# Optimization experiments

Measured on AMD Instinct MI355X. Metric: run time of the kernel, lower is better.

Reference implementation:

```python
import jax, jax.numpy as jnp
import numpy as np

B, S, N, D = 8, 2048, 512, 1024
MAX_W = 32  # fixed max span width (inclusive widths 0..MAX_W-1)
MASK_FILL = -1000.0


def setup_inputs() -> dict:
    key = jax.random.key(0)
    k1, k2, k3, k4 = jax.random.split(key, 4)
    sequence_tensor = jax.random.normal(k1, (B, S, D), dtype=jnp.float32)
    starts = jax.random.randint(k2, (B, N), 0, S - MAX_W)
    widths = jax.random.randint(k3, (B, N), 0, MAX_W)  # inclusive width = widths
    span_indices = jnp.stack([starts, starts + widths], axis=-1)  # (B, N, 2)
    att_w = jax.random.normal(k4, (D, 1), dtype=jnp.float32) * 0.02
    att_b = jnp.zeros((1,), dtype=jnp.float32)
    return {"sequence_tensor": sequence_tensor, "span_indices": span_indices,
            "att_w": att_w, "att_b": att_b}


def reference(sequence_tensor, span_indices, att_w, att_b):
    dtype = sequence_tensor.dtype
    starts = span_indices[..., 0]               # (B, N)
    ends = span_indices[..., 1]                 # (B, N), inclusive
    widths = ends - starts                      # (B, N)

    rng = jnp.arange(MAX_W)                     # (W,)
    raw_idx = ends[..., None] - rng             # (B, N, W), walks backward from end
    span_mask = (rng <= widths[..., None]) & (raw_idx >= 0)  # (B, N, W)
    idx = jnp.maximum(raw_idx, 0)               # relu on indices

    # global attention logits: (B, S, 1)
    logits = sequence_tensor @ att_w + att_b

    b, n = idx.shape[0], idx.shape[1]
    flat = idx.reshape(b, n * MAX_W)            # (B, N*W)
    # gather embeddings and logits over the time axis
    span_emb = jnp.take_along_axis(sequence_tensor, flat[..., None], axis=1)
    span_emb = span_emb.reshape(b, n, MAX_W, -1)              # (B, N, W, D)
    span_logits = jnp.take_along_axis(logits[..., 0], flat, axis=1)
    span_logits = span_logits.reshape(b, n, MAX_W)            # (B, N, W)

    # memory-efficient masked softmax: fill masked logits with -1000
    masked_logits = jnp.where(span_mask, span_logits, jnp.asarray(MASK_FILL, dtype))
    attn = jax.nn.softmax(masked_logits, axis=-1)             # (B, N, W)

    # weighted-sum pooling over span positions
    return jnp.einsum('bnw,bnwd->bnd', attn, span_emb)
```

## Files before the change

kernel.cpp:

```cpp
#include <hip/hip_runtime.h>
#include <hip/hip_bf16.h>

#define B 8
#define S 2048
#define N 512
#define D 1024
#define MAX_W 32
#define MASK_FILL -1000.0f

typedef float vfloat4 __attribute__((ext_vector_type(4)));

__device__ inline unsigned short f2bf(float f) {
    unsigned u = __float_as_uint(f);
    u += 0x7fff + ((u >> 16) & 1);
    return (unsigned short)(u >> 16);
}

__global__ __launch_bounds__(512) void prep_kernel(
    const float* __restrict__ seq,
    const float* __restrict__ att_w,
    const float* __restrict__ att_b,
    float* __restrict__ logits,
    unsigned short* __restrict__ seqh)
{
    const int row  = blockIdx.x * 8 + (threadIdx.x >> 6);
    const int lane = threadIdx.x & 63;

    const float4* rp = (const float4*)(seq + (size_t)row * D);
    const float4* wp = (const float4*)att_w;

    float4 a[4];
    float acc = 0.0f;
#pragma unroll
    for (int k = 0; k < 4; ++k) {
        a[k] = rp[lane + 64 * k];
        const float4 w = wp[lane + 64 * k];
        acc += a[k].x * w.x + a[k].y * w.y + a[k].z * w.z + a[k].w * w.w;
    }

    ushort4* hp = (ushort4*)(seqh + (size_t)row * D);
#pragma unroll
    for (int k = 0; k < 4; ++k) {
        ushort4 h;
        h.x = f2bf(a[k].x); h.y = f2bf(a[k].y);
        h.z = f2bf(a[k].z); h.w = f2bf(a[k].w);
        hp[lane + 64 * k] = h;
    }

#pragma unroll
    for (int off = 32; off > 0; off >>= 1)
        acc += __shfl_down(acc, off);
    if (lane == 0)
        logits[row] = acc + att_b[0];
}

__global__ __launch_bounds__(256) void pool_kernel(
    const unsigned short* __restrict__ seqh,
    const int*   __restrict__ spans,
    const float* __restrict__ logits,
    float* __restrict__ out)
{
    const int b    = blockIdx.x & 7;
    const int n    = blockIdx.x >> 3;
    const int span = b * N + n;

    const int start = spans[2 * span + 0];
    const int end   = spans[2 * span + 1];
    const int width = end - start;

    __shared__ float s_attn[MAX_W];
    __shared__ int   s_idx[MAX_W];
    __shared__ float s_part[128][9];

    const int tid  = threadIdx.x;
    const int c    = tid & 127;
    const int half = tid >> 7;

    if (tid < MAX_W) {
        const int w   = tid;
        const int raw = end - w;
        const bool valid = (w <= width) && (raw >= 0);
        const int idx = raw > start ? raw : start;
        const float l = valid ? logits[b * S + idx] : MASK_FILL;

        float m = l;
#pragma unroll
        for (int off = 16; off > 0; off >>= 1)
            m = fmaxf(m, __shfl_down(m, off, 32));
        m = __shfl(m, 0, 32);

        const float p = __expf(l - m);

        float sum = p;
#pragma unroll
        for (int off = 16; off > 0; off >>= 1)
            sum += __shfl_down(sum, off, 32);
        sum = __shfl(sum, 0, 32);

        s_attn[w] = p / sum;
        s_idx[w]  = idx;
    }
    __syncthreads();

    const unsigned short* sb = seqh + (size_t)b * S * D;

    float acc[8];
#pragma unroll
    for (int j = 0; j < 8; ++j) acc[j] = 0.0f;

    const int cnt  = width + 1;
    const int cnt8 = (cnt + 7) & ~7;

    for (int w = 0; w < cnt8; w += 8) {
        const int w0 = w + half;
        const float a0 = s_attn[w0 + 0];
        const float a1 = s_attn[w0 + 2];
        const float a2 = s_attn[w0 + 4];
        const float a3 = s_attn[w0 + 6];
        const int   i0 = s_idx[w0 + 0];
        const int   i1 = s_idx[w0 + 2];
        const int   i2 = s_idx[w0 + 4];
        const int   i3 = s_idx[w0 + 6];

        const uint4 q0 = ((const uint4*)(sb + (size_t)i0 * D))[c];
        const uint4 q1 = ((const uint4*)(sb + (size_t)i1 * D))[c];
        const uint4 q2 = ((const uint4*)(sb + (size_t)i2 * D))[c];
        const uint4 q3 = ((const uint4*)(sb + (size_t)i3 * D))[c];

#define BL(u) __uint_as_float((u) << 16)
#define BH(u) __uint_as_float((u) & 0xffff0000u)
        acc[0] += a0 * BL(q0.x) + a1 * BL(q1.x) + a2 * BL(q2.x) + a3 * BL(q3.x);
        acc[1] += a0 * BH(q0.x) + a1 * BH(q1.x) + a2 * BH(q2.x) + a3 * BH(q3.x);
        acc[2] += a0 * BL(q0.y) + a1 * BL(q1.y) + a2 * BL(q2.y) + a3 * BL(q3.y);
        acc[3] += a0 * BH(q0.y) + a1 * BH(q1.y) + a2 * BH(q2.y) + a3 * BH(q3.y);
        acc[4] += a0 * BL(q0.z) + a1 * BL(q1.z) + a2 * BL(q2.z) + a3 * BL(q3.z);
        acc[5] += a0 * BH(q0.z) + a1 * BH(q1.z) + a2 * BH(q2.z) + a3 * BH(q3.z);
        acc[6] += a0 * BL(q0.w) + a1 * BL(q1.w) + a2 * BL(q2.w) + a3 * BL(q3.w);
        acc[7] += a0 * BH(q0.w) + a1 * BH(q1.w) + a2 * BH(q2.w) + a3 * BH(q3.w);
#undef BL
#undef BH
    }

    if (half == 1) {
#pragma unroll
        for (int j = 0; j < 8; ++j) s_part[c][j] = acc[j];
    }
    __syncthreads();
    if (half == 0) {
#pragma unroll
        for (int j = 0; j < 8; ++j) acc[j] += s_part[c][j];

        vfloat4 va;
        va.x = acc[0]; va.y = acc[1]; va.z = acc[2]; va.w = acc[3];
        vfloat4* op = ((vfloat4*)(out + (size_t)span * D)) + 2 * c;
        __builtin_nontemporal_store(va, op);
        va.x = acc[4]; va.y = acc[5]; va.z = acc[6]; va.w = acc[7];
        __builtin_nontemporal_store(va, op + 1);
    }
}

extern "C" void kernel_launch(void* const* d_in, const int* in_sizes, int n_in,
                              void* d_out, int out_size, void* d_ws, size_t ws_size,
                              hipStream_t stream)
{
    const float* seq    = (const float*)d_in[0];
    const int*   spans  = (const int*)  d_in[1];
    const float* att_w  = (const float*)d_in[2];
    const float* att_b  = (const float*)d_in[3];

    float* out    = (float*)d_out;
    float* logits = (float*)d_ws;
    unsigned short* seqh =
        (unsigned short*)((char*)d_ws + (size_t)B * S * sizeof(float));

    prep_kernel<<<(B * S) / 8, 512, 0, stream>>>(seq, att_w, att_b,
                                                 logits, seqh);
    pool_kernel<<<B * N, 256, 0, stream>>>(seqh, spans, logits, out);
}
```

Before: 116.8 us.

## Switch staged rows to fp16 with packed dot2 accumulation and prefetch next rows

The staged copy of the sequence changes from bf16 to fp16, packed with cvt_pkrtz, and the pooling inner loop uses v_dot2 fp16 instructions on perm-packed pairs of rows with fp16-packed attention weights. Row offsets are precomputed as byte offsets in shared memory. The next group of four rows is software-prefetched before the current group is consumed. This aims to cut VALU work per element and hide gather latency, at the cost of lower-precision attention weights, a risk of fp16 range overflow, and extra registers.

Result: no change. 117.0 us (+0.2%).

```diff
diff --git a/kernel.cpp b/kernel.cpp
--- a/kernel.cpp
+++ b/kernel.cpp
@@ -1,5 +1,4 @@
 #include <hip/hip_runtime.h>
-#include <hip/hip_bf16.h>
 
 #define B 8
 #define S 2048
@@ -9,11 +8,27 @@
 #define MASK_FILL -1000.0f
 
 typedef float vfloat4 __attribute__((ext_vector_type(4)));
-
-__device__ inline unsigned short f2bf(float f) {
-    unsigned u = __float_as_uint(f);
-    u += 0x7fff + ((u >> 16) & 1);
-    return (unsigned short)(u >> 16);
+typedef __fp16 half2v __attribute__((ext_vector_type(2)));
+typedef unsigned int uint;
+
+__device__ inline uint pack_f16x2(float x, float y) {
+#if __has_builtin(__builtin_amdgcn_cvt_pkrtz)
+    half2v r = __builtin_amdgcn_cvt_pkrtz(x, y);
+    return __builtin_bit_cast(uint, r);
+#else
+    half2v r; r[0] = (__fp16)x; r[1] = (__fp16)y;
+    return __builtin_bit_cast(uint, r);
+#endif
+}
+
+__device__ inline float dot2(uint a, uint b, float c) {
+    half2v x = __builtin_bit_cast(half2v, a);
+    half2v y = __builtin_bit_cast(half2v, b);
+#if __has_builtin(__builtin_amdgcn_fdot2)
+    return __builtin_amdgcn_fdot2(x, y, c, false);
+#else
+    return c + (float)x[0] * (float)y[0] + (float)x[1] * (float)y[1];
+#endif
 }
 
 __global__ __launch_bounds__(512) void prep_kernel(
@@ -38,12 +53,12 @@
         acc += a[k].x * w.x + a[k].y * w.y + a[k].z * w.z + a[k].w * w.w;
     }
 
-    ushort4* hp = (ushort4*)(seqh + (size_t)row * D);
+    uint2* hp = (uint2*)(seqh + (size_t)row * D);
 #pragma unroll
     for (int k = 0; k < 4; ++k) {
-        ushort4 h;
-        h.x = f2bf(a[k].x); h.y = f2bf(a[k].y);
-        h.z = f2bf(a[k].z); h.w = f2bf(a[k].w);
+        uint2 h;
+        h.x = pack_f16x2(a[k].x, a[k].y);
+        h.y = pack_f16x2(a[k].z, a[k].w);
         hp[lane + 64 * k] = h;
     }
 
@@ -68,8 +83,8 @@
     const int end   = spans[2 * span + 1];
     const int width = end - start;
 
-    __shared__ float s_attn[MAX_W];
-    __shared__ int   s_idx[MAX_W];
+    __shared__ uint  s_ah2[MAX_W];
+    __shared__ uint  s_off[MAX_W];
     __shared__ float s_part[128][9];
 
     const int tid  = threadIdx.x;
@@ -97,12 +112,15 @@
             sum += __shfl_down(sum, off, 32);
         sum = __shfl(sum, 0, 32);
 
-        s_attn[w] = p / sum;
-        s_idx[w]  = idx;
+        const float at  = p / sum;
+        const float at2 = __shfl_down(at, 2, 32);
+        s_ah2[w] = pack_f16x2(at, at2);
+        s_off[w] = (uint)idx << 11;
     }
     __syncthreads();
 
-    const unsigned short* sb = seqh + (size_t)b * S * D;
+    const char* sb  = (const char*)seqh + (size_t)b * S * D * 2;
+    const uint  cvo = (uint)c * 16u;
 
     float acc[8];
 #pragma unroll
@@ -111,35 +129,46 @@
     const int cnt  = width + 1;
     const int cnt8 = (cnt + 7) & ~7;
 
+#define LDROW(OFF) (*(const uint4*)(sb + (OFF) + cvo))
+
+    uint4 q0 = LDROW(s_off[half + 0]);
+    uint4 q1 = LDROW(s_off[half + 2]);
+    uint4 q2 = LDROW(s_off[half + 4]);
+    uint4 q3 = LDROW(s_off[half + 6]);
+
     for (int w = 0; w < cnt8; w += 8) {
-        const int w0 = w + half;
-        const float a0 = s_attn[w0 + 0];
-        const float a1 = s_attn[w0 + 2];
-        const float a2 = s_attn[w0 + 4];
-        const float a3 = s_attn[w0 + 6];
-        const int   i0 = s_idx[w0 + 0];
-        const int   i1 = s_idx[w0 + 2];
-        const int   i2 = s_idx[w0 + 4];
-        const int   i3 = s_idx[w0 + 6];
-
-        const uint4 q0 = ((const uint4*)(sb + (size_t)i0 * D))[c];
-        const uint4 q1 = ((const uint4*)(sb + (size_t)i1 * D))[c];
-        const uint4 q2 = ((const uint4*)(sb + (size_t)i2 * D))[c];
-        const uint4 q3 = ((const uint4*)(sb + (size_t)i3 * D))[c];
-
-#define BL(u) __uint_as_float((u) << 16)
-#define BH(u) __uint_as_float((u) & 0xffff0000u)
-        acc[0] += a0 * BL(q0.x) + a1 * BL(q1.x) + a2 * BL(q2.x) + a3 * BL(q3.x);
-        acc[1] += a0 * BH(q0.x) + a1 * BH(q1.x) + a2 * BH(q2.x) + a3 * BH(q3.x);
-        acc[2] += a0 * BL(q0.y) + a1 * BL(q1.y) + a2 * BL(q2.y) + a3 * BL(q3.y);
-        acc[3] += a0 * BH(q0.y) + a1 * BH(q1.y) + a2 * BH(q2.y) + a3 * BH(q3.y);
-        acc[4] += a0 * BL(q0.z) + a1 * BL(q1.z) + a2 * BL(q2.z) + a3 * BL(q3.z);
-        acc[5] += a0 * BH(q0.z) + a1 * BH(q1.z) + a2 * BH(q2.z) + a3 * BH(q3.z);
-        acc[6] += a0 * BL(q0.w) + a1 * BL(q1.w) + a2 * BL(q2.w) + a3 * BL(q3.w);
-        acc[7] += a0 * BH(q0.w) + a1 * BH(q1.w) + a2 * BH(q2.w) + a3 * BH(q3.w);
-#undef BL
-#undef BH
-    }
+        const uint aA = s_ah2[w + half + 0];
+        const uint aB = s_ah2[w + half + 4];
+
+        uint4 n0, n1, n2, n3;
+        const bool more = (w + 8) < cnt8;
+        if (more) {
+            const int v0 = w + 8 + half;
+            n0 = LDROW(s_off[v0 + 0]);
+            n1 = LDROW(s_off[v0 + 2]);
+            n2 = LDROW(s_off[v0 + 4]);
+            n3 = LDROW(s_off[v0 + 6]);
+        }
+
+#define PAIR(qx, qy, ah, jlo, jhi)                                          \
+        acc[jlo] = dot2(ah, __builtin_amdgcn_perm(qy, qx, 0x05040100u),     \
+                        acc[jlo]);                                          \
+        acc[jhi] = dot2(ah, __builtin_amdgcn_perm(qy, qx, 0x07060302u),     \
+                        acc[jhi]);
+
+        PAIR(q0.x, q1.x, aA, 0, 1)
+        PAIR(q0.y, q1.y, aA, 2, 3)
+        PAIR(q0.z, q1.z, aA, 4, 5)
+        PAIR(q0.w, q1.w, aA, 6, 7)
+        PAIR(q2.x, q3.x, aB, 0, 1)
+        PAIR(q2.y, q3.y, aB, 2, 3)
+        PAIR(q2.z, q3.z, aB, 4, 5)
+        PAIR(q2.w, q3.w, aB, 6, 7)
+#undef PAIR
+
+        if (more) { q0 = n0; q1 = n1; q2 = n2; q3 = n3; }
+    }
+#undef LDROW
 
     if (half == 1) {
 #pragma unroll
```
